# Kernel optimization log

Hardware: AMD Instinct MI355X
Metric: run time of the kernel (lower is better)

The kernel has to match this reference:

```python
import jax, jax.numpy as jnp
import numpy as np

N_NODES = 20000
N_EDGES = 5000
STEPS = 50
INFECTION_RATE = 0.01
RECOVERY_RATE = 0.038
EDGE_DENSITY = 0.002  # ~10 hyperedges per node on average


def setup_inputs() -> dict:
    key = jax.random.key(0)
    k1, k2 = jax.random.split(key, 2)
    # initial SIR state per node: valid probability rows summing to 1
    u = jax.random.uniform(k1, (N_NODES, 3), dtype=jnp.float32)
    x = u / u.sum(axis=1, keepdims=True)
    # binary hypergraph incidence matrix (num_hyperedges, num_nodes)
    H = (jax.random.uniform(k2, (N_EDGES, N_NODES)) < EDGE_DENSITY).astype(jnp.float32)
    beta = jnp.full((N_NODES,), INFECTION_RATE, dtype=jnp.float32)
    gamma = jnp.full((N_NODES,), RECOVERY_RATE, dtype=jnp.float32)
    return {"x": x, "H": H, "beta": beta, "gamma": gamma, "steps": STEPS}


def reference(x, H, beta, gamma, steps):
    # x: (N, 3) [S, I, R] per node; H: (E, N) incidence.
    def step(state, _):
        S, I, R = state[:, 0], state[:, 1], state[:, 2]
        # hypergraph message passing: node -> hyperedge -> node
        new_cases = beta * (S * (H.T @ (H @ I)))
        new_recovery = gamma * I
        nxt = jnp.stack(
            [S - new_cases, I + new_cases - new_recovery, R + new_recovery], axis=1
        )
        nxt = jnp.maximum(nxt, 0.0)                       # clamp(min=0)
        nxt = nxt / nxt.sum(axis=1, keepdims=True)        # per-node row normalize
        return nxt, nxt

    _, traj = jax.lax.scan(step, x, None, length=steps - 1)
    # output[0] = initial state, then steps-1 simulated updates -> (steps, N, 3)
    return jnp.concatenate([x[None], traj], axis=0)
```

## Files before the change

### kernel.cpp

```cpp
#include <hip/hip_runtime.h>
#include <hip/hip_bf16.h>


#define EDGE_CAP 96
#define NODE_CAP 32

__global__ void zero_counts_kernel(int* edge_cnt, int* node_cnt, int n_edges, int n_nodes) {
    int i = blockIdx.x * blockDim.x + threadIdx.x;
    if (i < n_edges) edge_cnt[i] = 0;
    if (i < n_nodes) node_cnt[i] = 0;
}

__global__ void build_adjacency_kernel(const float* __restrict__ H,
                                       int* __restrict__ edge_cnt,
                                       int* __restrict__ edge_nodes,
                                       int* __restrict__ node_cnt,
                                       int* __restrict__ node_edges,
                                       int n_nodes) {
    const int e = blockIdx.x;
    const float* row = H + (size_t)e * n_nodes;
    const int n4 = n_nodes >> 2;
    const float4* row4 = (const float4*)row;
    for (int c4 = threadIdx.x; c4 < n4; c4 += blockDim.x) {
        float4 v = row4[c4];
        int cbase = c4 << 2;
        if (v.x != 0.0f) {
            int p = atomicAdd(&edge_cnt[e], 1);
            if (p < EDGE_CAP) edge_nodes[e * EDGE_CAP + p] = cbase;
            int q = atomicAdd(&node_cnt[cbase], 1);
            if (q < NODE_CAP) node_edges[cbase * NODE_CAP + q] = e;
        }
        if (v.y != 0.0f) {
            int c = cbase + 1;
            int p = atomicAdd(&edge_cnt[e], 1);
            if (p < EDGE_CAP) edge_nodes[e * EDGE_CAP + p] = c;
            int q = atomicAdd(&node_cnt[c], 1);
            if (q < NODE_CAP) node_edges[c * NODE_CAP + q] = e;
        }
        if (v.z != 0.0f) {
            int c = cbase + 2;
            int p = atomicAdd(&edge_cnt[e], 1);
            if (p < EDGE_CAP) edge_nodes[e * EDGE_CAP + p] = c;
            int q = atomicAdd(&node_cnt[c], 1);
            if (q < NODE_CAP) node_edges[c * NODE_CAP + q] = e;
        }
        if (v.w != 0.0f) {
            int c = cbase + 3;
            int p = atomicAdd(&edge_cnt[e], 1);
            if (p < EDGE_CAP) edge_nodes[e * EDGE_CAP + p] = c;
            int q = atomicAdd(&node_cnt[c], 1);
            if (q < NODE_CAP) node_edges[c * NODE_CAP + q] = e;
        }
    }
    if (threadIdx.x == 0) {
        for (int c = n4 << 2; c < n_nodes; ++c) {
            if (row[c] != 0.0f) {
                int p = atomicAdd(&edge_cnt[e], 1);
                if (p < EDGE_CAP) edge_nodes[e * EDGE_CAP + p] = c;
                int q = atomicAdd(&node_cnt[c], 1);
                if (q < NODE_CAP) node_edges[c * NODE_CAP + q] = e;
            }
        }
    }
}

__global__ void init_state_kernel(const float* __restrict__ x,
                                  float* __restrict__ S, float* __restrict__ I,
                                  float* __restrict__ R, float* __restrict__ out0,
                                  int n_nodes) {
    int n = blockIdx.x * blockDim.x + threadIdx.x;
    if (n >= n_nodes) return;
    float s = x[n * 3 + 0], iv = x[n * 3 + 1], r = x[n * 3 + 2];
    S[n] = s; I[n] = iv; R[n] = r;
    out0[n * 3 + 0] = s; out0[n * 3 + 1] = iv; out0[n * 3 + 2] = r;
}

__global__ void edge_sum_kernel(const int* __restrict__ edge_cnt,
                                const int* __restrict__ edge_nodes,
                                const float* __restrict__ I,
                                float* __restrict__ y, int n_edges) {
    int wavesPerBlock = blockDim.x >> 6;
    int e = blockIdx.x * wavesPerBlock + (threadIdx.x >> 6);
    int lane = threadIdx.x & 63;
    if (e >= n_edges) return;
    int cnt = min(edge_cnt[e], EDGE_CAP);
    float s = 0.0f;
    for (int i = lane; i < cnt; i += 64) s += I[edge_nodes[e * EDGE_CAP + i]];
    #pragma unroll
    for (int off = 32; off > 0; off >>= 1) s += __shfl_down(s, off, 64);
    if (lane == 0) y[e] = s;
}

__global__ void node_update_kernel(const int* __restrict__ node_cnt,
                                   const int* __restrict__ node_edges,
                                   const float* __restrict__ y,
                                   const float* __restrict__ beta,
                                   const float* __restrict__ gamma,
                                   float* __restrict__ S, float* __restrict__ I,
                                   float* __restrict__ R, float* __restrict__ out_t,
                                   int n_nodes) {
    int n = blockIdx.x * blockDim.x + threadIdx.x;
    if (n >= n_nodes) return;
    int cnt = min(node_cnt[n], NODE_CAP);
    float z = 0.0f;
    for (int i = 0; i < cnt; ++i) z += y[node_edges[n * NODE_CAP + i]];
    float s = S[n], iv = I[n], r = R[n];
    float nc = beta[n] * s * z;
    float nr = gamma[n] * iv;
    float s2 = fmaxf(s - nc, 0.0f);
    float i2 = fmaxf(iv + nc - nr, 0.0f);
    float r2 = fmaxf(r + nr, 0.0f);
    float inv = 1.0f / (s2 + i2 + r2);
    s2 *= inv; i2 *= inv; r2 *= inv;
    S[n] = s2; I[n] = i2; R[n] = r2;
    out_t[n * 3 + 0] = s2; out_t[n * 3 + 1] = i2; out_t[n * 3 + 2] = r2;
}

extern "C" void kernel_launch(void* const* d_in, const int* in_sizes, int n_in,
                              void* d_out, int out_size, void* d_ws, size_t ws_size,
                              hipStream_t stream) {
    const float* x     = (const float*)d_in[0];
    const float* H     = (const float*)d_in[1];
    const float* beta  = (const float*)d_in[2];
    const float* gamma = (const float*)d_in[3];
    float* out = (float*)d_out;

    const int n_nodes = in_sizes[0] / 3;
    const int n_edges = in_sizes[1] / n_nodes;
    const int steps   = out_size / in_sizes[0];

    char* ws = (char*)d_ws;
    int*   edge_cnt   = (int*)ws;                         ws += (size_t)n_edges * 4;
    int*   node_cnt   = (int*)ws;                         ws += (size_t)n_nodes * 4;
    int*   edge_nodes = (int*)ws;                         ws += (size_t)n_edges * EDGE_CAP * 4;
    int*   node_edges = (int*)ws;                         ws += (size_t)n_nodes * NODE_CAP * 4;
    float* y          = (float*)ws;                       ws += (size_t)n_edges * 4;
    float* S          = (float*)ws;                       ws += (size_t)n_nodes * 4;
    float* I          = (float*)ws;                       ws += (size_t)n_nodes * 4;
    float* R          = (float*)ws;                       ws += (size_t)n_nodes * 4;

    {
        int mx = max(n_edges, n_nodes);
        zero_counts_kernel<<<(mx + 255) / 256, 256, 0, stream>>>(edge_cnt, node_cnt, n_edges, n_nodes);
    }
    build_adjacency_kernel<<<n_edges, 256, 0, stream>>>(H, edge_cnt, edge_nodes,
                                                        node_cnt, node_edges, n_nodes);
    init_state_kernel<<<(n_nodes + 255) / 256, 256, 0, stream>>>(x, S, I, R, out, n_nodes);

    const int wavesPerBlock = 4;
    const int edgeGrid = (n_edges + wavesPerBlock - 1) / wavesPerBlock;
    for (int t = 1; t < steps; ++t) {
        edge_sum_kernel<<<edgeGrid, 256, 0, stream>>>(edge_cnt, edge_nodes, I, y, n_edges);
        node_update_kernel<<<(n_nodes + 255) / 256, 256, 0, stream>>>(
            node_cnt, node_edges, y, beta, gamma, S, I, R,
            out + (size_t)t * n_nodes * 3, n_nodes);
    }
}
```

Measured before the change: 1.069 ms.

## Fuse all SIR time steps into one persistent kernel with grid barriers

```diff
diff --git a/kernel.cpp b/kernel.cpp
--- a/kernel.cpp
+++ b/kernel.cpp
@@ -1,12 +1,15 @@
 #include <hip/hip_runtime.h>
-#include <hip/hip_bf16.h>
 
 
 #define EDGE_CAP 96
 #define NODE_CAP 32
+#define COOP_BLOCKS 64
+#define COOP_THREADS 1024
 
-__global__ void zero_counts_kernel(int* edge_cnt, int* node_cnt, int n_edges, int n_nodes) {
+__global__ void zero_counts_kernel(int* edge_cnt, int* node_cnt, unsigned* bar,
+                                   int n_edges, int n_nodes) {
     int i = blockIdx.x * blockDim.x + threadIdx.x;
+    if (i == 0) *bar = 0u;
     if (i < n_edges) edge_cnt[i] = 0;
     if (i < n_nodes) node_cnt[i] = 0;
 }
@@ -64,56 +67,75 @@
     }
 }
 
-__global__ void init_state_kernel(const float* __restrict__ x,
-                                  float* __restrict__ S, float* __restrict__ I,
-                                  float* __restrict__ R, float* __restrict__ out0,
-                                  int n_nodes) {
-    int n = blockIdx.x * blockDim.x + threadIdx.x;
-    if (n >= n_nodes) return;
-    float s = x[n * 3 + 0], iv = x[n * 3 + 1], r = x[n * 3 + 2];
-    S[n] = s; I[n] = iv; R[n] = r;
-    out0[n * 3 + 0] = s; out0[n * 3 + 1] = iv; out0[n * 3 + 2] = r;
+__device__ __forceinline__ void grid_sync(unsigned* bar, unsigned& target) {
+    __syncthreads();
+    target += (unsigned)gridDim.x;
+    if (threadIdx.x == 0) {
+        __builtin_amdgcn_fence(__ATOMIC_RELEASE, "agent");
+        atomicAdd(bar, 1u);
+        while (__hip_atomic_load(bar, __ATOMIC_RELAXED, __HIP_MEMORY_SCOPE_AGENT) < target)
+            __builtin_amdgcn_s_sleep(2);
+        __builtin_amdgcn_fence(__ATOMIC_ACQUIRE, "agent");
+    }
+    __syncthreads();
 }
 
-__global__ void edge_sum_kernel(const int* __restrict__ edge_cnt,
-                                const int* __restrict__ edge_nodes,
-                                const float* __restrict__ I,
-                                float* __restrict__ y, int n_edges) {
-    int wavesPerBlock = blockDim.x >> 6;
-    int e = blockIdx.x * wavesPerBlock + (threadIdx.x >> 6);
-    int lane = threadIdx.x & 63;
-    if (e >= n_edges) return;
-    int cnt = min(edge_cnt[e], EDGE_CAP);
-    float s = 0.0f;
-    for (int i = lane; i < cnt; i += 64) s += I[edge_nodes[e * EDGE_CAP + i]];
-    #pragma unroll
-    for (int off = 32; off > 0; off >>= 1) s += __shfl_down(s, off, 64);
-    if (lane == 0) y[e] = s;
-}
+__global__ __launch_bounds__(COOP_THREADS) void sir_steps_kernel(
+        const float* __restrict__ x,
+        const int* __restrict__ edge_cnt, const int* __restrict__ edge_nodes,
+        const int* __restrict__ node_cnt, const int* __restrict__ node_edges,
+        const float* __restrict__ beta, const float* __restrict__ gamma,
+        float* __restrict__ y, float* __restrict__ S, float* __restrict__ I,
+        float* __restrict__ R, float* __restrict__ out,
+        int n_nodes, int n_edges, int steps, unsigned* bar) {
+    const int tid = blockIdx.x * blockDim.x + threadIdx.x;
+    const int nthreads = gridDim.x * blockDim.x;
+    unsigned bar_target = 0;
 
-__global__ void node_update_kernel(const int* __restrict__ node_cnt,
-                                   const int* __restrict__ node_edges,
-                                   const float* __restrict__ y,
-                                   const float* __restrict__ beta,
-                                   const float* __restrict__ gamma,
-                                   float* __restrict__ S, float* __restrict__ I,
-                                   float* __restrict__ R, float* __restrict__ out_t,
-                                   int n_nodes) {
-    int n = blockIdx.x * blockDim.x + threadIdx.x;
-    if (n >= n_nodes) return;
-    int cnt = min(node_cnt[n], NODE_CAP);
-    float z = 0.0f;
-    for (int i = 0; i < cnt; ++i) z += y[node_edges[n * NODE_CAP + i]];
-    float s = S[n], iv = I[n], r = R[n];
-    float nc = beta[n] * s * z;
-    float nr = gamma[n] * iv;
-    float s2 = fmaxf(s - nc, 0.0f);
-    float i2 = fmaxf(iv + nc - nr, 0.0f);
-    float r2 = fmaxf(r + nr, 0.0f);
-    float inv = 1.0f / (s2 + i2 + r2);
-    s2 *= inv; i2 *= inv; r2 *= inv;
-    S[n] = s2; I[n] = i2; R[n] = r2;
-    out_t[n * 3 + 0] = s2; out_t[n * 3 + 1] = i2; out_t[n * 3 + 2] = r2;
+    for (int n = tid; n < n_nodes; n += nthreads) {
+        float s = x[n * 3 + 0], iv = x[n * 3 + 1], r = x[n * 3 + 2];
+        S[n] = s; I[n] = iv; R[n] = r;
+        out[n * 3 + 0] = s; out[n * 3 + 1] = iv; out[n * 3 + 2] = r;
+    }
+    grid_sync(bar, bar_target);
+
+    const int g  = tid >> 4;
+    const int gl = threadIdx.x & 15;
+    const int ngroups = nthreads >> 4;
+
+    for (int t = 1; t < steps; ++t) {
+        for (int e = g; e < n_edges; e += ngroups) {
+            int cnt = min(edge_cnt[e], EDGE_CAP);
+            const int* en = edge_nodes + e * EDGE_CAP;
+            float s = 0.0f;
+            for (int i = gl; i < cnt; i += 16) s += I[en[i]];
+            s += __shfl_down(s, 8, 16);
+            s += __shfl_down(s, 4, 16);
+            s += __shfl_down(s, 2, 16);
+            s += __shfl_down(s, 1, 16);
+            if (gl == 0) y[e] = s;
+        }
+        grid_sync(bar, bar_target);
+
+        float* out_t = out + (size_t)t * n_nodes * 3;
+        for (int n = tid; n < n_nodes; n += nthreads) {
+            int cnt = min(node_cnt[n], NODE_CAP);
+            const int* ne = node_edges + n * NODE_CAP;
+            float z = 0.0f;
+            for (int i = 0; i < cnt; ++i) z += y[ne[i]];
+            float s = S[n], iv = I[n], r = R[n];
+            float nc = beta[n] * s * z;
+            float nr = gamma[n] * iv;
+            float s2 = fmaxf(s - nc, 0.0f);
+            float i2 = fmaxf(iv + nc - nr, 0.0f);
+            float r2 = fmaxf(r + nr, 0.0f);
+            float inv = 1.0f / (s2 + i2 + r2);
+            s2 *= inv; i2 *= inv; r2 *= inv;
+            S[n] = s2; I[n] = i2; R[n] = r2;
+            out_t[n * 3 + 0] = s2; out_t[n * 3 + 1] = i2; out_t[n * 3 + 2] = r2;
+        }
+        if (t + 1 < steps) grid_sync(bar, bar_target);
+    }
 }
 
 extern "C" void kernel_launch(void* const* d_in, const int* in_sizes, int n_in,
@@ -130,6 +152,7 @@
     const int steps   = out_size / in_sizes[0];
 
     char* ws = (char*)d_ws;
+    unsigned* bar     = (unsigned*)ws;                    ws += 64;
     int*   edge_cnt   = (int*)ws;                         ws += (size_t)n_edges * 4;
     int*   node_cnt   = (int*)ws;                         ws += (size_t)n_nodes * 4;
     int*   edge_nodes = (int*)ws;                         ws += (size_t)n_edges * EDGE_CAP * 4;
@@ -141,18 +164,12 @@
 
     {
         int mx = max(n_edges, n_nodes);
-        zero_counts_kernel<<<(mx + 255) / 256, 256, 0, stream>>>(edge_cnt, node_cnt, n_edges, n_nodes);
+        zero_counts_kernel<<<(mx + 255) / 256, 256, 0, stream>>>(edge_cnt, node_cnt, bar,
+                                                                 n_edges, n_nodes);
     }
     build_adjacency_kernel<<<n_edges, 256, 0, stream>>>(H, edge_cnt, edge_nodes,
                                                         node_cnt, node_edges, n_nodes);
-    init_state_kernel<<<(n_nodes + 255) / 256, 256, 0, stream>>>(x, S, I, R, out, n_nodes);
-
-    const int wavesPerBlock = 4;
-    const int edgeGrid = (n_edges + wavesPerBlock - 1) / wavesPerBlock;
-    for (int t = 1; t < steps; ++t) {
-        edge_sum_kernel<<<edgeGrid, 256, 0, stream>>>(edge_cnt, edge_nodes, I, y, n_edges);
-        node_update_kernel<<<(n_nodes + 255) / 256, 256, 0, stream>>>(
-            node_cnt, node_edges, y, beta, gamma, S, I, R,
-            out + (size_t)t * n_nodes * 3, n_nodes);
-    }
+    sir_steps_kernel<<<COOP_BLOCKS, COOP_THREADS, 0, stream>>>(
+        x, edge_cnt, edge_nodes, node_cnt, node_edges, beta, gamma,
+        y, S, I, R, out, n_nodes, n_edges, steps, bar);
 }
```

New measurement: 1.628 ms. +52.2%, slower.
